# Kernel tuning notes

Hardware: AMD Instinct MI355X
Metric: run time of the kernel (lower is better)

Reference implementation:

```python
import jax, jax.numpy as jnp
import numpy as np

B, T, E, H = 512, 256, 384, 64

def setup_inputs() -> dict:
    key = jax.random.key(0)
    k1, k2, k3, k4 = jax.random.split(key, 4)
    scale = 1.0 / np.sqrt(E)
    return {
        "x":  jax.random.normal(k1, (B, T, E), dtype=jnp.float32),
        "Wq": jax.random.normal(k2, (E, H), dtype=jnp.float32) * scale,
        "Wk": jax.random.normal(k3, (E, H), dtype=jnp.float32) * scale,
        "Wv": jax.random.normal(k4, (E, H), dtype=jnp.float32) * scale,
    }

def reference(x, Wq, Wk, Wv):
    # single-head causal self-attention (dropout in eval mode / identity)
    q = jnp.einsum('bte,eh->bth', x, Wq)
    k = jnp.einsum('bte,eh->bth', x, Wk)
    v = jnp.einsum('bte,eh->bth', x, Wv)
    d = q.shape[-1]
    wei = jnp.einsum('bqh,bkh->bqk', q, k) * (d ** -0.5)   # [B,T,T]
    T_ = x.shape[1]
    causal = jnp.tril(jnp.ones((T_, T_), dtype=bool))
    wei = jnp.where(causal[None, :, :], wei, -jnp.inf)
    wei = jax.nn.softmax(wei, axis=-1)
    out = jnp.einsum('bqk,bkh->bqh', wei, v)               # [B,T,H]
    return out
```

## Files before the change

### kernel.cpp

```cpp
#include <hip/hip_runtime.h>

typedef __attribute__((ext_vector_type(4)))  float f32x4;
typedef __attribute__((ext_vector_type(16))) float f32x16;
typedef __attribute__((ext_vector_type(8)))  short s16x8;
typedef __attribute__((ext_vector_type(4)))  short s16x4;


__device__ inline short f2bf(float f){
  unsigned u = __float_as_uint(f);
  u = u + 0x7fffu + ((u >> 16) & 1u);
  return (short)(u >> 16);
}

__device__ __forceinline__ void gld16(const void* g, void* l){
  __builtin_amdgcn_global_load_lds((const __attribute__((address_space(1))) void*)g,
                                   (__attribute__((address_space(3))) void*)l, 16, 0, 0);
}

__global__ void wt_prep_kernel(const float* __restrict__ Wq, const float* __restrict__ Wk,
                               const float* __restrict__ Wv, short* __restrict__ Wt){
  int o = blockIdx.x * 256 + threadIdx.x;
  if (o >= 192*384) return;
  int n = o / 384, k = o - n*384;
  const float* W = (n < 64) ? Wq : (n < 128) ? Wk : Wv;
  Wt[o] = f2bf(W[k*64 + (n & 63)]);
}

__global__ __launch_bounds__(512, 4) void qkv2_kernel(const float* __restrict__ x,
    const short* __restrict__ Wt, short* __restrict__ Qg,
    short* __restrict__ Kg, short* __restrict__ Vg){
  __shared__ __align__(16) float xs[2][128][32];

  const int tid  = threadIdx.x;
  const int w    = tid >> 6, lane = tid & 63;
  const int l31  = lane & 31, hh = lane >> 5;
  const int wn   = w >> 2,  wt = w & 3;
  const int b    = blockIdx.x >> 1;
  const int t0   = (blockIdx.x & 1) << 7;

  const char* xbase = (const char*)x + ((long)b*256 + t0)*1536;

  auto stage = [&](int kt, int buf){
    #pragma unroll
    for (int i2 = 0; i2 < 2; ++i2){
      const int ii = w*2 + i2;
      const int r  = ii*8 + (lane >> 3);
      const char* src = xbase + (long)r*1536 + kt*128
                      + ((((lane & 7) ^ (lane >> 3)) << 4));
      gld16(src, (char*)&xs[buf][ii*8][0]);
    }
  };

  f32x16 acc[3];
  #pragma unroll
  for (int c = 0; c < 3; ++c)
    #pragma unroll
    for (int i = 0; i < 16; ++i) acc[c][i] = 0.0f;

  const int swr = (l31 & 7) << 4;
  const short* wrow = Wt + (wn*96 + l31)*384;

  stage(0, 0);
  __syncthreads();

  for (int kt = 0; kt < 12; ++kt){
    if (kt < 11) stage(kt + 1, (kt + 1) & 1);

    const char* bp = (const char*)&xs[kt & 1][wt*32 + l31][0];
    #pragma unroll
    for (int s = 0; s < 2; ++s){
      const int c0 = s*64 + hh*32;
      f32x4 a0 = *(const f32x4*)(bp + ((c0     ) ^ swr));
      f32x4 a1 = *(const f32x4*)(bp + ((c0 + 16) ^ swr));
      s16x8 bx;
      bx[0]=f2bf(a0[0]); bx[1]=f2bf(a0[1]); bx[2]=f2bf(a0[2]); bx[3]=f2bf(a0[3]);
      bx[4]=f2bf(a1[0]); bx[5]=f2bf(a1[1]); bx[6]=f2bf(a1[2]); bx[7]=f2bf(a1[3]);

      const short* wp = wrow + kt*32 + s*16 + hh*8;
      s16x8 w0 = *(const s16x8*)(wp);
      s16x8 w1 = *(const s16x8*)(wp + 32*384);
      s16x8 w2 = *(const s16x8*)(wp + 64*384);
      if (wn == 0){
        acc[0] = __builtin_amdgcn_mfma_f32_32x32x16_bf16(w0, bx, acc[0], 0, 0, 0);
        acc[1] = __builtin_amdgcn_mfma_f32_32x32x16_bf16(w1, bx, acc[1], 0, 0, 0);
        acc[2] = __builtin_amdgcn_mfma_f32_32x32x16_bf16(w2, bx, acc[2], 0, 0, 0);
      } else {
        acc[0] = __builtin_amdgcn_mfma_f32_32x32x16_bf16(w0, bx, acc[0], 0, 0, 0);
        acc[1] = __builtin_amdgcn_mfma_f32_32x32x16_bf16(bx, w1, acc[1], 0, 0, 0);
        acc[2] = __builtin_amdgcn_mfma_f32_32x32x16_bf16(bx, w2, acc[2], 0, 0, 0);
      }
    }
    __syncthreads();
  }

  const int tl = t0 + wt*32 + l31;
  short* Qb = Qg + (long)b*16384;
  char*  Kb = (char*)(Kg + (long)b*16384);
  char*  Vb = (char*)(Vg + (long)b*16384);

  if (wn == 0){
    #pragma unroll
    for (int c = 0; c < 2; ++c)
      #pragma unroll
      for (int g = 0; g < 4; ++g){
        s16x4 v;
        #pragma unroll
        for (int j = 0; j < 4; ++j) v[j] = f2bf(acc[c][4*g + j]);
        *(s16x4*)(Qb + (long)tl*64 + c*32 + 8*g + 4*hh) = v;
      }
    const int swk = (tl & 7) << 4;
    #pragma unroll
    for (int g = 0; g < 4; ++g){
      s16x4 v;
      #pragma unroll
      for (int j = 0; j < 4; ++j) v[j] = f2bf(acc[2][4*g + j]);
      *(s16x4*)(Kb + (long)tl*128 + ((16*g + 8*hh) ^ swk)) = v;
    }
  } else {
    const int swk = (tl & 7) << 4;
    #pragma unroll
    for (int g = 0; g < 4; ++g){
      s16x4 v;
      #pragma unroll
      for (int j = 0; j < 4; ++j) v[j] = f2bf(acc[0][4*g + j]);
      *(s16x4*)(Kb + (long)tl*128 + ((64 + 16*g + 8*hh) ^ swk)) = v;
    }
    #pragma unroll
    for (int c = 1; c < 3; ++c){
      const int h   = (c - 1)*32 + l31;
      const int swv = (h & 7) << 4;
      #pragma unroll
      for (int g = 0; g < 4; ++g){
        const int tb = t0 + wt*32 + 8*g + 4*hh;
        s16x4 v;
        #pragma unroll
        for (int j = 0; j < 4; ++j) v[j] = f2bf(acc[c][4*g + j]);
        *(s16x4*)(Vb + (long)h*512 + ((tb*2) ^ swv)) = v;
      }
    }
  }
}

__global__ __launch_bounds__(512, 4) void attn_kernel(const short* __restrict__ Qg,
    const short* __restrict__ Kg, const short* __restrict__ Vg,
    float* __restrict__ out){
  __shared__ __align__(16) short Ks[16384];
  __shared__ __align__(16) short Vts[16384];
  __shared__ __align__(16) short Pp[8][16*40];

  const int tid  = threadIdx.x;
  const int w    = tid >> 6, lane = tid & 63;
  const int l15  = lane & 15, quad = lane >> 4;
  const int b    = blockIdx.x;

  const short* Qb = Qg + (long)b*16384;
  const int F0 = w, F1 = 15 - w;
  s16x8 qA0 = *(const s16x8*)(Qb + (F0*16 + l15)*64 + quad*8);
  s16x8 qA1 = *(const s16x8*)(Qb + (F0*16 + l15)*64 + 32 + quad*8);
  s16x8 qB0 = *(const s16x8*)(Qb + (F1*16 + l15)*64 + quad*8);
  s16x8 qB1 = *(const s16x8*)(Qb + (F1*16 + l15)*64 + 32 + quad*8);

  const char* Kb = (const char*)(Kg + (long)b*16384);
  const char* Vb = (const char*)(Vg + (long)b*16384);
  {
    const int base = w*4096;
    #pragma unroll
    for (int i = 0; i < 4; ++i){
      gld16(Kb + base + i*1024 + lane*16, (char*)Ks  + base + i*1024);
      gld16(Vb + base + i*1024 + lane*16, (char*)Vts + base + i*1024);
    }
  }
  __syncthreads();

  float* ob = out + (long)b*256*64;
  short* Pw = Pp[w];
  const int swz = (l15 & 7) << 4;

  auto attend = [&](int F, s16x8 qf0, s16x8 qf1){
    const int qb = F*16;
    const int NF = F + 1;
    const int NS = (NF + 1) >> 1;

    f32x4 sc[16];
    #pragma unroll
    for (int f = 0; f < 16; ++f){
      f32x4 a;
      #pragma unroll
      for (int r = 0; r < 4; ++r) a[r] = 0.0f;
      if (f < NF){
        const char* kp = (const char*)Ks + (f*16 + l15)*128;
        s16x8 k0v = *(const s16x8*)(kp + ((quad*16)      ^ swz));
        s16x8 k1v = *(const s16x8*)(kp + ((64 + quad*16) ^ swz));
        a = __builtin_amdgcn_mfma_f32_16x16x32_bf16(qf0, k0v, a, 0, 0, 0);
        a = __builtin_amdgcn_mfma_f32_16x16x32_bf16(qf1, k1v, a, 0, 0, 0);
      }
      sc[f] = a;
    }

    float mx[4], sm[4];
    #pragma unroll
    for (int r = 0; r < 4; ++r) mx[r] = -3.0e38f;
    #pragma unroll
    for (int f = 0; f < 16; ++f){
      if (f < NF){
        const int key = f*16 + l15;
        #pragma unroll
        for (int r = 0; r < 4; ++r){
          const int qg = qb + quad*4 + r;
          float s = sc[f][r] * 0.125f;
          s = (key <= qg) ? s : -1.0e30f;
          sc[f][r] = s;
          mx[r] = fmaxf(mx[r], s);
        }
      }
    }
    #pragma unroll
    for (int r = 0; r < 4; ++r){
      #pragma unroll
      for (int off = 1; off < 16; off <<= 1) mx[r] = fmaxf(mx[r], __shfl_xor(mx[r], off, 16));
    }
    #pragma unroll
    for (int r = 0; r < 4; ++r) sm[r] = 0.0f;
    #pragma unroll
    for (int f = 0; f < 16; ++f){
      if (f < NF){
        #pragma unroll
        for (int r = 0; r < 4; ++r){
          float p = exp2f((sc[f][r] - mx[r]) * 1.44269504f);
          sc[f][r] = p;
          sm[r] += p;
        }
      }
    }
    #pragma unroll
    for (int r = 0; r < 4; ++r){
      #pragma unroll
      for (int off = 1; off < 16; off <<= 1) sm[r] += __shfl_xor(sm[r], off, 16);
    }

    f32x4 o[4];
    #pragma unroll
    for (int h0 = 0; h0 < 4; ++h0)
      #pragma unroll
      for (int r = 0; r < 4; ++r) o[h0][r] = 0.0f;

    #pragma unroll
    for (int ks = 0; ks < 8; ++ks){
      if (ks < NS){
        #pragma unroll
        for (int fi = 0; fi < 2; ++fi){
          const int f = 2*ks + fi;
          #pragma unroll
          for (int r = 0; r < 4; ++r){
            short v = 0;
            if (f < NF) v = f2bf(sc[f][r]);
            Pw[(quad*4 + r)*40 + fi*16 + l15] = v;
          }
        }
        s16x8 pf = *(const s16x8*)(Pw + l15*40 + quad*8);
        #pragma unroll
        for (int h0 = 0; h0 < 4; ++h0){
          const char* vp = (const char*)Vts + (h0*16 + l15)*512;
          s16x8 vf = *(const s16x8*)(vp + ((ks*64 + quad*16) ^ swz));
          o[h0] = __builtin_amdgcn_mfma_f32_16x16x32_bf16(pf, vf, o[h0], 0, 0, 0);
        }
      }
    }

    #pragma unroll
    for (int r = 0; r < 4; ++r){
      const float inv = 1.0f / sm[r];
      #pragma unroll
      for (int h0 = 0; h0 < 4; ++h0)
        ob[(qb + quad*4 + r)*64 + h0*16 + l15] = o[h0][r] * inv;
    }
  };
  attend(F0, qA0, qA1);
  attend(F1, qB0, qB1);
}

__global__ __launch_bounds__(512, 4) void fused2_kernel(const float* __restrict__ x,
                             const short* __restrict__ Wt, float* __restrict__ out){
  __shared__ __align__(16) char  KsB[32768];
  __shared__ __align__(16) char  VtsB[32768];
  __shared__ __align__(16) short Pp[8][16*40];

  const int tid  = threadIdx.x;
  const int w    = tid >> 6, lane = tid & 63;
  const int l15  = lane & 15, quad = lane >> 4;
  const int b    = blockIdx.x;

  const float* xb = x + (long)b*256*384;
  const int F0 = w, F1 = 15 - w;

  s16x8 qA0, qA1, qB0, qB1;

  auto project = [&](int r0, s16x8& qf0, s16x8& qf1){
    f32x4 aq[4], ak[4], av[4];
    #pragma unroll
    for (int c = 0; c < 4; ++c)
      #pragma unroll
      for (int i = 0; i < 4; ++i){ aq[c][i]=0.f; ak[c][i]=0.f; av[c][i]=0.f; }

    const float* xr = xb + (long)(r0 + l15)*384;
    #pragma unroll 2
    for (int kt = 0; kt < 12; ++kt){
      const int k0 = kt*32 + quad*8;
      float4 a0 = *(const float4*)(xr + k0);
      float4 a1 = *(const float4*)(xr + k0 + 4);
      s16x8 bx;
      bx[0]=f2bf(a0.x); bx[1]=f2bf(a0.y); bx[2]=f2bf(a0.z); bx[3]=f2bf(a0.w);
      bx[4]=f2bf(a1.x); bx[5]=f2bf(a1.y); bx[6]=f2bf(a1.z); bx[7]=f2bf(a1.w);
      #pragma unroll
      for (int c = 0; c < 4; ++c){
        s16x8 wq = *(const s16x8*)(Wt + (c*16 + l15)*384 + k0);
        aq[c] = __builtin_amdgcn_mfma_f32_16x16x32_bf16(wq, bx, aq[c], 0, 0, 0);
      }
      #pragma unroll
      for (int c = 0; c < 4; ++c){
        s16x8 wk = *(const s16x8*)(Wt + ((c+4)*16 + l15)*384 + k0);
        ak[c] = __builtin_amdgcn_mfma_f32_16x16x32_bf16(wk, bx, ak[c], 0, 0, 0);
      }
      #pragma unroll
      for (int c = 0; c < 4; ++c){
        s16x8 wv = *(const s16x8*)(Wt + ((c+8)*16 + l15)*384 + k0);
        av[c] = __builtin_amdgcn_mfma_f32_16x16x32_bf16(bx, wv, av[c], 0, 0, 0);
      }
    }

    char* krow = KsB + (r0 + l15)*128;
    const int swzr = (l15 & 7) << 4;

    #pragma unroll
    for (int c = 0; c < 4; ++c){
      s16x4 v;
      #pragma unroll
      for (int i = 0; i < 4; ++i) v[i] = f2bf(aq[c][i]);
      *(s16x4*)(krow + ((c*32 + quad*8) ^ swzr)) = v;
    }
    asm volatile("s_waitcnt lgkmcnt(0)" ::: "memory");
    qf0 = *(const s16x8*)(krow + ((quad*16)      ^ swzr));
    qf1 = *(const s16x8*)(krow + ((64 + quad*16) ^ swzr));
    asm volatile("s_waitcnt lgkmcnt(0)" ::: "memory");

    #pragma unroll
    for (int c = 0; c < 4; ++c){
      s16x4 v;
      #pragma unroll
      for (int i = 0; i < 4; ++i) v[i] = f2bf(ak[c][i]);
      *(s16x4*)(krow + ((c*32 + quad*8) ^ swzr)) = v;
    }
    #pragma unroll
    for (int c = 0; c < 4; ++c){
      const int h = c*16 + l15;
      s16x4 v;
      #pragma unroll
      for (int i = 0; i < 4; ++i) v[i] = f2bf(av[c][i]);
      *(s16x4*)(VtsB + h*512 + (((r0 + quad*4)*2) ^ ((h & 7) << 4))) = v;
    }
  };

  project(F0*16, qA0, qA1);
  project(F1*16, qB0, qB1);

  __syncthreads();

  float* ob = out + (long)b*256*64;
  short* Pw = Pp[w];
  const int swz = (l15 & 7) << 4;

  auto attend = [&](int F, s16x8 qf0, s16x8 qf1){
    const int qb = F*16;
    const int NF = F + 1;
    const int NS = (NF + 1) >> 1;

    f32x4 sc[16];
    #pragma unroll
    for (int f = 0; f < 16; ++f){
      f32x4 a;
      #pragma unroll
      for (int r = 0; r < 4; ++r) a[r] = 0.0f;
      if (f < NF){
        const char* kp = KsB + (f*16 + l15)*128;
        s16x8 k0v = *(const s16x8*)(kp + ((quad*16)      ^ swz));
        s16x8 k1v = *(const s16x8*)(kp + ((64 + quad*16) ^ swz));
        a = __builtin_amdgcn_mfma_f32_16x16x32_bf16(qf0, k0v, a, 0, 0, 0);
        a = __builtin_amdgcn_mfma_f32_16x16x32_bf16(qf1, k1v, a, 0, 0, 0);
      }
      sc[f] = a;
    }

    float mx[4], sm[4];
    #pragma unroll
    for (int r = 0; r < 4; ++r) mx[r] = -3.0e38f;
    #pragma unroll
    for (int f = 0; f < 16; ++f){
      if (f < NF){
        const int key = f*16 + l15;
        #pragma unroll
        for (int r = 0; r < 4; ++r){
          const int qg = qb + quad*4 + r;
          float s = sc[f][r] * 0.125f;
          s = (key <= qg) ? s : -1.0e30f;
          sc[f][r] = s;
          mx[r] = fmaxf(mx[r], s);
        }
      }
    }
    #pragma unroll
    for (int r = 0; r < 4; ++r){
      #pragma unroll
      for (int off = 1; off < 16; off <<= 1) mx[r] = fmaxf(mx[r], __shfl_xor(mx[r], off, 16));
    }
    #pragma unroll
    for (int r = 0; r < 4; ++r) sm[r] = 0.0f;
    #pragma unroll
    for (int f = 0; f < 16; ++f){
      if (f < NF){
        #pragma unroll
        for (int r = 0; r < 4; ++r){
          float p = exp2f((sc[f][r] - mx[r]) * 1.44269504f);
          sc[f][r] = p;
          sm[r] += p;
        }
      }
    }
    #pragma unroll
    for (int r = 0; r < 4; ++r){
      #pragma unroll
      for (int off = 1; off < 16; off <<= 1) sm[r] += __shfl_xor(sm[r], off, 16);
    }

    f32x4 o[4];
    #pragma unroll
    for (int h0 = 0; h0 < 4; ++h0)
      #pragma unroll
      for (int r = 0; r < 4; ++r) o[h0][r] = 0.0f;

    #pragma unroll
    for (int ks = 0; ks < 8; ++ks){
      if (ks < NS){
        #pragma unroll
        for (int fi = 0; fi < 2; ++fi){
          const int f = 2*ks + fi;
          #pragma unroll
          for (int r = 0; r < 4; ++r){
            short v = 0;
            if (f < NF) v = f2bf(sc[f][r]);
            Pw[(quad*4 + r)*40 + fi*16 + l15] = v;
          }
        }
        s16x8 pf = *(const s16x8*)(Pw + l15*40 + quad*8);
        #pragma unroll
        for (int h0 = 0; h0 < 4; ++h0){
          const char* vp = VtsB + (h0*16 + l15)*512;
          s16x8 vf = *(const s16x8*)(vp + ((ks*64 + quad*16) ^ swz));
          o[h0] = __builtin_amdgcn_mfma_f32_16x16x32_bf16(pf, vf, o[h0], 0, 0, 0);
        }
      }
    }

    #pragma unroll
    for (int r = 0; r < 4; ++r){
      const float inv = 1.0f / sm[r];
      #pragma unroll
      for (int h0 = 0; h0 < 4; ++h0)
        ob[(qb + quad*4 + r)*64 + h0*16 + l15] = o[h0][r] * inv;
    }
  };

  attend(F0, qA0, qA1);
  attend(F1, qB0, qB1);
}

extern "C" void kernel_launch(void* const* d_in, const int* in_sizes, int n_in,
                              void* d_out, int out_size, void* d_ws, size_t ws_size,
                              hipStream_t stream){
  const float* x  = (const float*)d_in[0];
  const float* Wq = (const float*)d_in[1];
  const float* Wk = (const float*)d_in[2];
  const float* Wv = (const float*)d_in[3];
  float* out = (float*)d_out;

  short* Wt = (short*)d_ws;
  const size_t need = 147456 + 3ull*16777216ull;

  hipLaunchKernelGGL(wt_prep_kernel, dim3(288), dim3(256), 0, stream, Wq, Wk, Wv, Wt);
  if (ws_size >= need){
    short* Qg = (short*)((char*)d_ws + 147456);
    short* Kg = Qg + 8388608;
    short* Vg = Kg + 8388608;
    hipLaunchKernelGGL(qkv2_kernel, dim3(1024), dim3(512), 0, stream, x, Wt, Qg, Kg, Vg);
    hipLaunchKernelGGL(attn_kernel, dim3(512),  dim3(512), 0, stream, Qg, Kg, Vg, out);
  } else {
    hipLaunchKernelGGL(fused2_kernel, dim3(512), dim3(512), 0, stream, x, Wt, out);
  }
}
```

Baseline: 364.2 us.

## Deepen QKV projection pipeline with 4-stage LDS ring and register-prefetched weights

The QKV projection kernel now uses a four-buffer LDS ring, with x tiles staged three k-steps ahead. Weight fragments are double-buffered in registers and prefetched one step ahead, and a vmcnt-based wait plus one barrier per step replaces the old double-buffer sync. Float-to-bf16 packing switches to the hardware v_cvt_pk_bf16_f32 instruction. The aim is to hide global load latency and cut conversion ALU work, at the cost of twice the LDS per block and more registers, which may lower occupancy.

```diff
diff --git a/kernel.cpp b/kernel.cpp
--- a/kernel.cpp
+++ b/kernel.cpp
@@ -10,6 +10,15 @@
   unsigned u = __float_as_uint(f);
   u = u + 0x7fffu + ((u >> 16) & 1u);
   return (short)(u >> 16);
+}
+
+__device__ __forceinline__ s16x8 pack8(f32x4 a0, f32x4 a1){
+  union { s16x8 v; unsigned u[4]; } r;
+  asm("v_cvt_pk_bf16_f32 %0, %1, %2" : "=v"(r.u[0]) : "v"(a0[0]), "v"(a0[1]));
+  asm("v_cvt_pk_bf16_f32 %0, %1, %2" : "=v"(r.u[1]) : "v"(a0[2]), "v"(a0[3]));
+  asm("v_cvt_pk_bf16_f32 %0, %1, %2" : "=v"(r.u[2]) : "v"(a1[0]), "v"(a1[1]));
+  asm("v_cvt_pk_bf16_f32 %0, %1, %2" : "=v"(r.u[3]) : "v"(a1[2]), "v"(a1[3]));
+  return r.v;
 }
 
 __device__ __forceinline__ void gld16(const void* g, void* l){
@@ -26,10 +35,10 @@
   Wt[o] = f2bf(W[k*64 + (n & 63)]);
 }
 
-__global__ __launch_bounds__(512, 4) void qkv2_kernel(const float* __restrict__ x,
+__global__ __launch_bounds__(512, 4) void qkv3_kernel(const float* __restrict__ x,
     const short* __restrict__ Wt, short* __restrict__ Qg,
     short* __restrict__ Kg, short* __restrict__ Vg){
-  __shared__ __align__(16) float xs[2][128][32];
+  __shared__ __align__(16) float xs[4][128][32];
 
   const int tid  = threadIdx.x;
   const int w    = tid >> 6, lane = tid & 63;
@@ -60,37 +69,73 @@
   const int swr = (l31 & 7) << 4;
   const short* wrow = Wt + (wn*96 + l31)*384;
 
+  auto loadWt = [&](int kt, s16x8& a0, s16x8& a1, s16x8& a2,
+                            s16x8& b0, s16x8& b1, s16x8& b2){
+    const short* wp0 = wrow + kt*32 + hh*8;
+    a0 = *(const s16x8*)(wp0);
+    a1 = *(const s16x8*)(wp0 + 32*384);
+    a2 = *(const s16x8*)(wp0 + 64*384);
+    const short* wp1 = wp0 + 16;
+    b0 = *(const s16x8*)(wp1);
+    b1 = *(const s16x8*)(wp1 + 32*384);
+    b2 = *(const s16x8*)(wp1 + 64*384);
+  };
+
+  auto compute = [&](int kt, s16x8 w0a, s16x8 w1a, s16x8 w2a,
+                             s16x8 w0b, s16x8 w1b, s16x8 w2b){
+    const char* bp = (const char*)&xs[kt & 3][wt*32 + l31][0];
+    {
+      f32x4 a0 = *(const f32x4*)(bp + ((hh*32)      ^ swr));
+      f32x4 a1 = *(const f32x4*)(bp + ((hh*32 + 16) ^ swr));
+      s16x8 bx = pack8(a0, a1);
+      if (wn == 0){
+        acc[0] = __builtin_amdgcn_mfma_f32_32x32x16_bf16(w0a, bx, acc[0], 0, 0, 0);
+        acc[1] = __builtin_amdgcn_mfma_f32_32x32x16_bf16(w1a, bx, acc[1], 0, 0, 0);
+        acc[2] = __builtin_amdgcn_mfma_f32_32x32x16_bf16(w2a, bx, acc[2], 0, 0, 0);
+      } else {
+        acc[0] = __builtin_amdgcn_mfma_f32_32x32x16_bf16(w0a, bx, acc[0], 0, 0, 0);
+        acc[1] = __builtin_amdgcn_mfma_f32_32x32x16_bf16(bx, w1a, acc[1], 0, 0, 0);
+        acc[2] = __builtin_amdgcn_mfma_f32_32x32x16_bf16(bx, w2a, acc[2], 0, 0, 0);
+      }
+    }
+    {
+      f32x4 a0 = *(const f32x4*)(bp + ((64 + hh*32)      ^ swr));
+      f32x4 a1 = *(const f32x4*)(bp + ((64 + hh*32 + 16) ^ swr));
+      s16x8 bx = pack8(a0, a1);
+      if (wn == 0){
+        acc[0] = __builtin_amdgcn_mfma_f32_32x32x16_bf16(w0b, bx, acc[0], 0, 0, 0);
+        acc[1] = __builtin_amdgcn_mfma_f32_32x32x16_bf16(w1b, bx, acc[1], 0, 0, 0);
+        acc[2] = __builtin_amdgcn_mfma_f32_32x32x16_bf16(w2b, bx, acc[2], 0, 0, 0);
+      } else {
+        acc[0] = __builtin_amdgcn_mfma_f32_32x32x16_bf16(w0b, bx, acc[0], 0, 0, 0);
+        acc[1] = __builtin_amdgcn_mfma_f32_32x32x16_bf16(bx, w1b, acc[1], 0, 0, 0);
+        acc[2] = __builtin_amdgcn_mfma_f32_32x32x16_bf16(bx, w2b, acc[2], 0, 0, 0);
+      }
+    }
+  };
+
+  s16x8 A0,A1,A2,A3,A4,A5, B0,B1,B2,B3,B4,B5;
+
   stage(0, 0);
-  __syncthreads();
-
-  for (int kt = 0; kt < 12; ++kt){
-    if (kt < 11) stage(kt + 1, (kt + 1) & 1);
-
-    const char* bp = (const char*)&xs[kt & 1][wt*32 + l31][0];
-    #pragma unroll
-    for (int s = 0; s < 2; ++s){
-      const int c0 = s*64 + hh*32;
-      f32x4 a0 = *(const f32x4*)(bp + ((c0     ) ^ swr));
-      f32x4 a1 = *(const f32x4*)(bp + ((c0 + 16) ^ swr));
-      s16x8 bx;
-      bx[0]=f2bf(a0[0]); bx[1]=f2bf(a0[1]); bx[2]=f2bf(a0[2]); bx[3]=f2bf(a0[3]);
-      bx[4]=f2bf(a1[0]); bx[5]=f2bf(a1[1]); bx[6]=f2bf(a1[2]); bx[7]=f2bf(a1[3]);
-
-      const short* wp = wrow + kt*32 + s*16 + hh*8;
-      s16x8 w0 = *(const s16x8*)(wp);
-      s16x8 w1 = *(const s16x8*)(wp + 32*384);
-      s16x8 w2 = *(const s16x8*)(wp + 64*384);
-      if (wn == 0){
-        acc[0] = __builtin_amdgcn_mfma_f32_32x32x16_bf16(w0, bx, acc[0], 0, 0, 0);
-        acc[1] = __builtin_amdgcn_mfma_f32_32x32x16_bf16(w1, bx, acc[1], 0, 0, 0);
-        acc[2] = __builtin_amdgcn_mfma_f32_32x32x16_bf16(w2, bx, acc[2], 0, 0, 0);
-      } else {
-        acc[0] = __builtin_amdgcn_mfma_f32_32x32x16_bf16(w0, bx, acc[0], 0, 0, 0);
-        acc[1] = __builtin_amdgcn_mfma_f32_32x32x16_bf16(bx, w1, acc[1], 0, 0, 0);
-        acc[2] = __builtin_amdgcn_mfma_f32_32x32x16_bf16(bx, w2, acc[2], 0, 0, 0);
-      }
-    }
-    __syncthreads();
+  stage(1, 1);
+  loadWt(0, A0, A1, A2, A3, A4, A5);
+  stage(2, 2);
+
+  auto step = [&](int kt,
+                  s16x8& c0, s16x8& c1, s16x8& c2, s16x8& c3, s16x8& c4, s16x8& c5,
+                  s16x8& n0, s16x8& n1, s16x8& n2, s16x8& n3, s16x8& n4, s16x8& n5){
+    asm volatile("s_waitcnt vmcnt(10)" ::: "memory");
+    __builtin_amdgcn_s_barrier();
+    __builtin_amdgcn_sched_barrier(0);
+    if (kt < 11) loadWt(kt + 1, n0, n1, n2, n3, n4, n5);
+    if (kt < 9)  stage(kt + 3, (kt + 3) & 3);
+    compute(kt, c0, c1, c2, c3, c4, c5);
+  };
+
+  #pragma unroll 1
+  for (int k2 = 0; k2 < 6; ++k2){
+    step(2*k2,     A0,A1,A2,A3,A4,A5,  B0,B1,B2,B3,B4,B5);
+    step(2*k2 + 1, B0,B1,B2,B3,B4,B5,  A0,A1,A2,A3,A4,A5);
   }
 
   const int tl = t0 + wt*32 + l31;
@@ -490,7 +535,7 @@
     short* Qg = (short*)((char*)d_ws + 147456);
     short* Kg = Qg + 8388608;
     short* Vg = Kg + 8388608;
-    hipLaunchKernelGGL(qkv2_kernel, dim3(1024), dim3(512), 0, stream, x, Wt, Qg, Kg, Vg);
+    hipLaunchKernelGGL(qkv3_kernel, dim3(1024), dim3(512), 0, stream, x, Wt, Qg, Kg, Vg);
     hipLaunchKernelGGL(attn_kernel, dim3(512),  dim3(512), 0, stream, Qg, Kg, Vg, out);
   } else {
     hipLaunchKernelGGL(fused2_kernel, dim3(512), dim3(512), 0, stream, x, Wt, out);
```

After: 353.1 us. 3.0% less time.

## Restructure QKV projection to per-wave 16-row tiles with pre-swizzled weight fragments

Applied to the files above, without the earlier changes.

Rewrites the QKV projection kernel so each wave owns 16 token rows and computes all 192 output columns with 16x16x32 MFMAs. Weights are pre-packed by a new prep kernel into a per-lane fragment layout, so each wave loads them with one coalesced vector load per tile. The x tile is staged per wave in LDS, which replaces the block-wide __syncthreads with a per-wave vmcnt wait. bf16 conversion of x now uses packed v_cvt_pk_bf16_f32 instructions. The cost is more accumulator registers and redundant weight reads by every wave.

```diff
diff --git a/kernel.cpp b/kernel.cpp
--- a/kernel.cpp
+++ b/kernel.cpp
@@ -1,7 +1,6 @@
 #include <hip/hip_runtime.h>
 
 typedef __attribute__((ext_vector_type(4)))  float f32x4;
-typedef __attribute__((ext_vector_type(16))) float f32x16;
 typedef __attribute__((ext_vector_type(8)))  short s16x8;
 typedef __attribute__((ext_vector_type(4)))  short s16x4;
 
@@ -10,6 +9,15 @@
   unsigned u = __float_as_uint(f);
   u = u + 0x7fffu + ((u >> 16) & 1u);
   return (short)(u >> 16);
+}
+
+__device__ __forceinline__ s16x8 pack8(f32x4 a0, f32x4 a1){
+  union { s16x8 v; unsigned u[4]; } r;
+  asm("v_cvt_pk_bf16_f32 %0, %1, %2" : "=v"(r.u[0]) : "v"(a0[0]), "v"(a0[1]));
+  asm("v_cvt_pk_bf16_f32 %0, %1, %2" : "=v"(r.u[1]) : "v"(a0[2]), "v"(a0[3]));
+  asm("v_cvt_pk_bf16_f32 %0, %1, %2" : "=v"(r.u[2]) : "v"(a1[0]), "v"(a1[1]));
+  asm("v_cvt_pk_bf16_f32 %0, %1, %2" : "=v"(r.u[3]) : "v"(a1[2]), "v"(a1[3]));
+  return r.v;
 }
 
 __device__ __forceinline__ void gld16(const void* g, void* l){
@@ -26,118 +34,107 @@
   Wt[o] = f2bf(W[k*64 + (n & 63)]);
 }
 
-__global__ __launch_bounds__(512, 4) void qkv2_kernel(const float* __restrict__ x,
-    const short* __restrict__ Wt, short* __restrict__ Qg,
+__global__ void wt_prep2_kernel(const float* __restrict__ Wq, const float* __restrict__ Wk,
+                                const float* __restrict__ Wv, short* __restrict__ Wt2){
+  int f = blockIdx.x * 256 + threadIdx.x;
+  if (f >= 9216) return;
+  int Bq = f >> 6, lane = f & 63;
+  int kt = Bq / 12, c = Bq - kt*12;
+  int col = c*16 + (lane & 15);
+  int k0  = kt*32 + (lane >> 4)*8;
+  const float* W = (col < 64) ? Wq : (col < 128) ? Wk : Wv;
+  int cc = col & 63;
+  short* dst = Wt2 + (long)f*8;
+  #pragma unroll
+  for (int j = 0; j < 8; ++j) dst[j] = f2bf(W[(k0 + j)*64 + cc]);
+}
+
+__global__ __launch_bounds__(512, 4) void qkv4_kernel(const float* __restrict__ x,
+    const short* __restrict__ Wt2, short* __restrict__ Qg,
     short* __restrict__ Kg, short* __restrict__ Vg){
-  __shared__ __align__(16) float xs[2][128][32];
+  __shared__ __align__(16) char xlds[8][2][2048];
 
   const int tid  = threadIdx.x;
   const int w    = tid >> 6, lane = tid & 63;
-  const int l31  = lane & 31, hh = lane >> 5;
-  const int wn   = w >> 2,  wt = w & 3;
+  const int l15  = lane & 15, quad = lane >> 4;
   const int b    = blockIdx.x >> 1;
   const int t0   = (blockIdx.x & 1) << 7;
-
-  const char* xbase = (const char*)x + ((long)b*256 + t0)*1536;
+  const int r0   = t0 + w*16;
+
+  const char* xbase = (const char*)x + ((long)b*256 + r0)*1536;
 
   auto stage = [&](int kt, int buf){
     #pragma unroll
-    for (int i2 = 0; i2 < 2; ++i2){
-      const int ii = w*2 + i2;
-      const int r  = ii*8 + (lane >> 3);
-      const char* src = xbase + (long)r*1536 + kt*128
-                      + ((((lane & 7) ^ (lane >> 3)) << 4));
-      gld16(src, (char*)&xs[buf][ii*8][0]);
+    for (int i = 0; i < 2; ++i){
+      const char* src = xbase + (long)(i*8 + (lane >> 3))*1536 + kt*128
+                      + ((((lane & 7) ^ (lane >> 3))) << 4);
+      gld16(src, &xlds[w][buf][i*1024]);
     }
   };
 
-  f32x16 acc[3];
+  f32x4 acc[12];
   #pragma unroll
-  for (int c = 0; c < 3; ++c)
-    #pragma unroll
-    for (int i = 0; i < 16; ++i) acc[c][i] = 0.0f;
-
-  const int swr = (l31 & 7) << 4;
-  const short* wrow = Wt + (wn*96 + l31)*384;
+  for (int c = 0; c < 12; ++c)
+    #pragma unroll
+    for (int i = 0; i < 4; ++i) acc[c][i] = 0.0f;
+
+  const short* wlane = Wt2 + lane*8;
+  const int xsw = (l15 & 7) << 4;
 
   stage(0, 0);
-  __syncthreads();
-
+
+  #pragma unroll 2
   for (int kt = 0; kt < 12; ++kt){
+    s16x8 wf[12];
+    #pragma unroll
+    for (int c = 0; c < 12; ++c)
+      wf[c] = *(const s16x8*)(wlane + (kt*12 + c)*512);
+    __builtin_amdgcn_sched_barrier(0);
     if (kt < 11) stage(kt + 1, (kt + 1) & 1);
-
-    const char* bp = (const char*)&xs[kt & 1][wt*32 + l31][0];
-    #pragma unroll
-    for (int s = 0; s < 2; ++s){
-      const int c0 = s*64 + hh*32;
-      f32x4 a0 = *(const f32x4*)(bp + ((c0     ) ^ swr));
-      f32x4 a1 = *(const f32x4*)(bp + ((c0 + 16) ^ swr));
-      s16x8 bx;
-      bx[0]=f2bf(a0[0]); bx[1]=f2bf(a0[1]); bx[2]=f2bf(a0[2]); bx[3]=f2bf(a0[3]);
-      bx[4]=f2bf(a1[0]); bx[5]=f2bf(a1[1]); bx[6]=f2bf(a1[2]); bx[7]=f2bf(a1[3]);
-
-      const short* wp = wrow + kt*32 + s*16 + hh*8;
-      s16x8 w0 = *(const s16x8*)(wp);
-      s16x8 w1 = *(const s16x8*)(wp + 32*384);
-      s16x8 w2 = *(const s16x8*)(wp + 64*384);
-      if (wn == 0){
-        acc[0] = __builtin_amdgcn_mfma_f32_32x32x16_bf16(w0, bx, acc[0], 0, 0, 0);
-        acc[1] = __builtin_amdgcn_mfma_f32_32x32x16_bf16(w1, bx, acc[1], 0, 0, 0);
-        acc[2] = __builtin_amdgcn_mfma_f32_32x32x16_bf16(w2, bx, acc[2], 0, 0, 0);
-      } else {
-        acc[0] = __builtin_amdgcn_mfma_f32_32x32x16_bf16(w0, bx, acc[0], 0, 0, 0);
-        acc[1] = __builtin_amdgcn_mfma_f32_32x32x16_bf16(bx, w1, acc[1], 0, 0, 0);
-        acc[2] = __builtin_amdgcn_mfma_f32_32x32x16_bf16(bx, w2, acc[2], 0, 0, 0);
-      }
-    }
-    __syncthreads();
-  }
-
-  const int tl = t0 + wt*32 + l31;
+    asm volatile("s_waitcnt vmcnt(2)" ::: "memory");
+    __builtin_amdgcn_sched_barrier(0);
+    const char* bp = &xlds[w][kt & 1][0];
+    f32x4 a0 = *(const f32x4*)(bp + l15*128 + ((quad*32)      ^ xsw));
+    f32x4 a1 = *(const f32x4*)(bp + l15*128 + ((quad*32 + 16) ^ xsw));
+    s16x8 bx = pack8(a0, a1);
+    #pragma unroll
+    for (int c = 0; c < 8; ++c)
+      acc[c] = __builtin_amdgcn_mfma_f32_16x16x32_bf16(wf[c], bx, acc[c], 0, 0, 0);
+    #pragma unroll
+    for (int c = 8; c < 12; ++c)
+      acc[c] = __builtin_amdgcn_mfma_f32_16x16x32_bf16(bx, wf[c], acc[c], 0, 0, 0);
+  }
+
+  const int tr = r0 + l15;
   short* Qb = Qg + (long)b*16384;
   char*  Kb = (char*)(Kg + (long)b*16384);
   char*  Vb = (char*)(Vg + (long)b*16384);
 
-  if (wn == 0){
-    #pragma unroll
-    for (int c = 0; c < 2; ++c)
-      #pragma unroll
-      for (int g = 0; g < 4; ++g){
-        s16x4 v;
-        #pragma unroll
-        for (int j = 0; j < 4; ++j) v[j] = f2bf(acc[c][4*g + j]);
-        *(s16x4*)(Qb + (long)tl*64 + c*32 + 8*g + 4*hh) = v;
-      }
-    const int swk = (tl & 7) << 4;
-    #pragma unroll
-    for (int g = 0; g < 4; ++g){
+  #pragma unroll
+  for (int c = 0; c < 4; ++c){
+    s16x4 v;
+    #pragma unroll
+    for (int i = 0; i < 4; ++i) v[i] = f2bf(acc[c][i]);
+    *(s16x4*)(Qb + (long)tr*64 + c*16 + quad*4) = v;
+  }
+  {
+    const int swk = (tr & 7) << 4;
+    #pragma unroll
+    for (int c = 4; c < 8; ++c){
       s16x4 v;
       #pragma unroll
-      for (int j = 0; j < 4; ++j) v[j] = f2bf(acc[2][4*g + j]);
-      *(s16x4*)(Kb + (long)tl*128 + ((16*g + 8*hh) ^ swk)) = v;
-    }
-  } else {
-    const int swk = (tl & 7) << 4;
-    #pragma unroll
-    for (int g = 0; g < 4; ++g){
-      s16x4 v;
-      #pragma unroll
-      for (int j = 0; j < 4; ++j) v[j] = f2bf(acc[0][4*g + j]);
-      *(s16x4*)(Kb + (long)tl*128 + ((64 + 16*g + 8*hh) ^ swk)) = v;
-    }
-    #pragma unroll
-    for (int c = 1; c < 3; ++c){
-      const int h   = (c - 1)*32 + l31;
-      const int swv = (h & 7) << 4;
-      #pragma unroll
-      for (int g = 0; g < 4; ++g){
-        const int tb = t0 + wt*32 + 8*g + 4*hh;
-        s16x4 v;
-        #pragma unroll
-        for (int j = 0; j < 4; ++j) v[j] = f2bf(acc[c][4*g + j]);
-        *(s16x4*)(Vb + (long)h*512 + ((tb*2) ^ swv)) = v;
-      }
-    }
+      for (int i = 0; i < 4; ++i) v[i] = f2bf(acc[c][i]);
+      *(s16x4*)(Kb + (long)tr*128 + (((c - 4)*32 + quad*8) ^ swk)) = v;
+    }
+  }
+  #pragma unroll
+  for (int c = 8; c < 12; ++c){
+    const int h   = (c - 8)*16 + l15;
+    const int swv = (h & 7) << 4;
+    s16x4 v;
+    #pragma unroll
+    for (int i = 0; i < 4; ++i) v[i] = f2bf(acc[c][i]);
+    *(s16x4*)(Vb + (long)h*512 + (((r0 + quad*4)*2) ^ swv)) = v;
   }
 }
 
@@ -485,14 +482,15 @@
   short* Wt = (short*)d_ws;
   const size_t need = 147456 + 3ull*16777216ull;
 
-  hipLaunchKernelGGL(wt_prep_kernel, dim3(288), dim3(256), 0, stream, Wq, Wk, Wv, Wt);
   if (ws_size >= need){
     short* Qg = (short*)((char*)d_ws + 147456);
     short* Kg = Qg + 8388608;
     short* Vg = Kg + 8388608;
-    hipLaunchKernelGGL(qkv2_kernel, dim3(1024), dim3(512), 0, stream, x, Wt, Qg, Kg, Vg);
+    hipLaunchKernelGGL(wt_prep2_kernel, dim3(36), dim3(256), 0, stream, Wq, Wk, Wv, Wt);
+    hipLaunchKernelGGL(qkv4_kernel, dim3(1024), dim3(512), 0, stream, x, Wt, Qg, Kg, Vg);
     hipLaunchKernelGGL(attn_kernel, dim3(512),  dim3(512), 0, stream, Qg, Kg, Vg, out);
   } else {
+    hipLaunchKernelGGL(wt_prep_kernel, dim3(288), dim3(256), 0, stream, Wq, Wk, Wv, Wt);
     hipLaunchKernelGGL(fused2_kernel, dim3(512), dim3(512), 0, stream, x, Wt, out);
   }
 }
```

New measurement: 356.8 us. 1.02x faster.
